# Optimization experiments

Hardware: AMD Instinct MI355X
Metric: run time of the kernel (lower is better)

## Reference

```python
import jax, jax.numpy as jnp
import numpy as np

B, S, D, H, F = 2, 4096, 512, 8, 2048
DH = D // H
EPS = 1e-3  # keras LayerNormalization default epsilon


def _ln(x, g, b):
    m = jnp.mean(x, axis=-1, keepdims=True)
    v = jnp.mean(jnp.square(x - m), axis=-1, keepdims=True)
    return (x - m) * jax.lax.rsqrt(v + EPS) * g + b


def setup_inputs() -> dict:
    key = jax.random.key(0)
    ks = jax.random.split(key, 8)
    sd = 0.02
    x = jax.random.normal(ks[0], (B, S, D), jnp.float32)
    # 0/1 additive-style mask: 1 above the diagonal -> masked via mask * -1e9 (causal)
    mask = jnp.triu(jnp.ones((S, S), jnp.float32), k=1)[None, None]
    return {
        "x": x,
        "mask": mask,
        "wq": jax.random.normal(ks[1], (D, D), jnp.float32) * sd, "bq": jnp.zeros((D,), jnp.float32),
        "wk": jax.random.normal(ks[2], (D, D), jnp.float32) * sd, "bk": jnp.zeros((D,), jnp.float32),
        "wv": jax.random.normal(ks[3], (D, D), jnp.float32) * sd, "bv": jnp.zeros((D,), jnp.float32),
        "wo": jax.random.normal(ks[4], (D, D), jnp.float32) * sd, "bo": jnp.zeros((D,), jnp.float32),
        "ln1_g": jnp.ones((D,), jnp.float32), "ln1_b": jnp.zeros((D,), jnp.float32),
        "w1": jax.random.normal(ks[5], (D, F), jnp.float32) * sd, "b1": jnp.zeros((F,), jnp.float32),
        "w2": jax.random.normal(ks[6], (F, D), jnp.float32) * sd, "b2": jnp.zeros((D,), jnp.float32),
        "ln2_g": jnp.ones((D,), jnp.float32), "ln2_b": jnp.zeros((D,), jnp.float32),
    }


def reference(x, mask, wq, bq, wk, bk, wv, bv, wo, bo, ln1_g, ln1_b,
              w1, b1, w2, b2, ln2_g, ln2_b):
    # --- multi-head attention (dropout = identity at inference) ---
    def heads(t, w, b):  # [B,S,D] -> [B,H,S,DH]
        return (t @ w + b).reshape(B, S, H, DH).transpose(0, 2, 1, 3)
    q = heads(x, wq, bq)
    k = heads(x, wk, bk)
    v = heads(x, wv, bv)
    scores = jnp.einsum("bhqd,bhkd->bhqk", q, k) / jnp.sqrt(jnp.float32(DH))
    scores = scores + mask * (-1e9)
    attn = jax.nn.softmax(scores, axis=-1)            # [B,H,S,S] -- the 1 GB tensor
    ctx = jnp.einsum("bhqk,bhkd->bhqd", attn, v)       # [B,H,S,DH]
    ctx = ctx.transpose(0, 2, 1, 3).reshape(B, S, D)
    attn_out = ctx @ wo + bo
    # --- residual + LN 1 ---
    y = _ln(x + attn_out, ln1_g, ln1_b)
    # --- pointwise FFN (Conv1D kernel_size=1 == Dense) ---
    ffn = jax.nn.relu(y @ w1 + b1) @ w2 + b2
    # --- residual + LN 2 ---
    return _ln(y + ffn, ln2_g, ln2_b)
```

## Files before the change

### kernel.cpp

```cpp
#include <hip/hip_runtime.h>
#include <hip/hip_bf16.h>
#include <math.h>

#define Bb 2
#define Ss 4096
#define Dd 512
#define Hh 8
#define Ff 2048
#define Mm 8192
#define QT3 1536
#define KVB 128

typedef float  f32x4  __attribute__((ext_vector_type(4)));
typedef short  bf16x8 __attribute__((ext_vector_type(8)));

__device__ __forceinline__ ushort f2bf(float f) {
  union { float f; uint u; } c; c.f = f;
  uint u = c.u;
  uint r = (u + 0x7fffu + ((u >> 16) & 1u)) >> 16;
  return (ushort)r;
}

__device__ __forceinline__ ushort f2bf_rhu(float f) {
  union { float f; uint u; } c; c.f = f;
  return (ushort)((c.u + 0x8000u) >> 16);
}

__device__ __forceinline__ void gload_lds16(const ushort* g, ushort* l) {
  __builtin_amdgcn_global_load_lds(
      (const __attribute__((address_space(1))) void*)g,
      (__attribute__((address_space(3))) void*)l, 16, 0, 0);
}

template<bool OUTBF, bool RELU>
__global__ __launch_bounds__(256) void gemm_mfma(const ushort* __restrict__ A,
                                                 const ushort* __restrict__ Bt,
                                                 const float* __restrict__ bias,
                                                 void* __restrict__ Cout,
                                                 int M, int N, int K) {
  __shared__ __align__(16) ushort As[128 * 32];
  __shared__ __align__(16) ushort Bs[128 * 32];
  const int t = threadIdx.x;
  const int w = t >> 6, lane = t & 63;
  const int lrow = lane & 15, lhi = lane >> 4;
  const int bm = blockIdx.y * 128, bn = blockIdx.x * 128;
  const int wm = (w >> 1) * 64, wn = (w & 1) * 64;
  const int sr = t >> 2, sc = (t & 3) * 8;

  f32x4 acc[4][4];
#pragma unroll
  for (int i = 0; i < 4; ++i)
#pragma unroll
    for (int j = 0; j < 4; ++j) acc[i][j] = (f32x4)(0.f);

  const ushort* Ap = A  + (size_t)(bm + sr) * K + sc;
  const ushort* Bp = Bt + (size_t)(bn + sr) * K + sc;
  const size_t rowK64 = (size_t)64 * K;
  ushort* AsW0 = As + w * 512;
  ushort* AsW1 = As + 2048 + w * 512;
  ushort* BsW0 = Bs + w * 512;
  ushort* BsW1 = Bs + 2048 + w * 512;

  for (int k0 = 0; k0 < K; k0 += 32) {
    __syncthreads();
    gload_lds16(Ap + k0,          AsW0);
    gload_lds16(Ap + rowK64 + k0, AsW1);
    gload_lds16(Bp + k0,          BsW0);
    gload_lds16(Bp + rowK64 + k0, BsW1);
    __syncthreads();
    bf16x8 af[4], bfr[4];
#pragma unroll
    for (int i = 0; i < 4; ++i)
      af[i] = *(const bf16x8*)&As[(wm + i * 16 + lrow) * 32 + lhi * 8];
#pragma unroll
    for (int j = 0; j < 4; ++j)
      bfr[j] = *(const bf16x8*)&Bs[(wn + j * 16 + lrow) * 32 + lhi * 8];
#pragma unroll
    for (int i = 0; i < 4; ++i)
#pragma unroll
      for (int j = 0; j < 4; ++j)
        acc[i][j] = __builtin_amdgcn_mfma_f32_16x16x32_bf16(af[i], bfr[j], acc[i][j], 0, 0, 0);
  }

  float bvs[4];
#pragma unroll
  for (int j = 0; j < 4; ++j) bvs[j] = bias[bn + wn + j * 16 + lrow];

#pragma unroll
  for (int i = 0; i < 4; ++i)
#pragma unroll
    for (int r = 0; r < 4; ++r) {
      const int row = bm + wm + i * 16 + lhi * 4 + r;
#pragma unroll
      for (int j = 0; j < 4; ++j) {
        float val = acc[i][j][r] + bvs[j];
        if (RELU) val = fmaxf(val, 0.f);
        const size_t idx = (size_t)row * N + bn + wn + j * 16 + lrow;
        if (OUTBF) ((ushort*)Cout)[idx] = f2bf(val);
        else       ((float*)Cout)[idx]  = val;
      }
    }
}

__global__ __launch_bounds__(256, 3) void flash_attn_mfma(const ushort* __restrict__ qkv,
                                                          ushort* __restrict__ ctx) {
  __shared__ __align__(16) ushort Ks[128][72];
  __shared__ __align__(16) ushort Vt[64][136];
  __shared__ __align__(16) ushort Ps[4][16][136];

  const int t = threadIdx.x;
  const int w = t >> 6, lane = t & 63;
  const int lrow = lane & 15, lhi = lane >> 4;
  const int qt = (int)(gridDim.x - 1 - blockIdx.x);
  const int bh = blockIdx.y;
  const int bb = bh >> 3, hh = bh & 7;
  const int q0 = qt * 64;
  const size_t baseq = (size_t)bb * Ss * QT3 + hh * 64;
  const ushort* qp = qkv + baseq;
  const ushort* kp = qkv + baseq + 512;
  const ushort* vp = qkv + baseq + 1024;

  const int krow = t >> 1, kd0 = (t & 1) * 32;
  const int vk0 = lane * 2, vd0 = w * 16;

  bf16x8 qa[2];
  {
    const ushort* qsrc = qp + (size_t)(q0 + w * 16 + lrow) * QT3;
    qa[0] = *(const bf16x8*)(qsrc + lhi * 8);
    qa[1] = *(const bf16x8*)(qsrc + 32 + lhi * 8);
  }

  float m2[4], lsum[4];
  f32x4 oacc[4];
#pragma unroll
  for (int r = 0; r < 4; ++r) { m2[r] = -INFINITY; lsum[r] = 0.f; }
#pragma unroll
  for (int g = 0; g < 4; ++g) oacc[g] = (f32x4)(0.f);

  const int nt = (qt + 2) >> 1;
  const float C2 = 0.18033688f;

  bf16x8 kr[4], va[2], vb[2];
  {
    const ushort* ksrc = kp + (size_t)krow * QT3 + kd0;
#pragma unroll
    for (int j = 0; j < 4; ++j) kr[j] = *(const bf16x8*)(ksrc + j * 8);
    const ushort* vsrc = vp + (size_t)vk0 * QT3 + vd0;
    va[0] = *(const bf16x8*)(vsrc);
    va[1] = *(const bf16x8*)(vsrc + 8);
    vb[0] = *(const bf16x8*)(vsrc + QT3);
    vb[1] = *(const bf16x8*)(vsrc + QT3 + 8);
  }

  for (int kt = 0; kt < nt; ++kt) {
    const int j0 = kt * KVB;

    __syncthreads();
#pragma unroll
    for (int j = 0; j < 4; ++j)
      *(bf16x8*)&Ks[krow][kd0 + j * 8] = kr[j];
#pragma unroll
    for (int i = 0; i < 8; ++i) {
      uint p0 = (uint)(ushort)va[0][i] | ((uint)(ushort)vb[0][i] << 16);
      uint p1 = (uint)(ushort)va[1][i] | ((uint)(ushort)vb[1][i] << 16);
      *(uint*)&Vt[vd0 + i][vk0]     = p0;
      *(uint*)&Vt[vd0 + 8 + i][vk0] = p1;
    }
    __syncthreads();

    if (kt + 1 < nt) {
      const int jn = j0 + KVB;
      const ushort* ksrc = kp + (size_t)(jn + krow) * QT3 + kd0;
#pragma unroll
      for (int j = 0; j < 4; ++j) kr[j] = *(const bf16x8*)(ksrc + j * 8);
      const ushort* vsrc = vp + (size_t)(jn + vk0) * QT3 + vd0;
      va[0] = *(const bf16x8*)(vsrc);
      va[1] = *(const bf16x8*)(vsrc + 8);
      vb[0] = *(const bf16x8*)(vsrc + QT3);
      vb[1] = *(const bf16x8*)(vsrc + QT3 + 8);
    }

    f32x4 sacc[8];
#pragma unroll
    for (int g = 0; g < 8; ++g) sacc[g] = (f32x4)(0.f);
#pragma unroll
    for (int g = 0; g < 8; ++g)
#pragma unroll
      for (int kk = 0; kk < 2; ++kk) {
        bf16x8 kb = *(const bf16x8*)&Ks[g * 16 + lrow][kk * 32 + lhi * 8];
        sacc[g] = __builtin_amdgcn_mfma_f32_16x16x32_bf16(qa[kk], kb, sacc[g], 0, 0, 0);
      }

    if (j0 + KVB - 1 > q0) {
#pragma unroll
      for (int g = 0; g < 8; ++g) {
        const int kcol = j0 + g * 16 + lrow;
#pragma unroll
        for (int r = 0; r < 4; ++r) {
          const int qrow = q0 + w * 16 + lhi * 4 + r;
          if (kcol > qrow) sacc[g][r] = -1e30f;
        }
      }
    }

    float pm[4];
#pragma unroll
    for (int r = 0; r < 4; ++r) {
      float m01 = fmaxf(sacc[0][r], sacc[1][r]);
      float m23 = fmaxf(sacc[2][r], sacc[3][r]);
      float m45 = fmaxf(sacc[4][r], sacc[5][r]);
      float m67 = fmaxf(sacc[6][r], sacc[7][r]);
      pm[r] = fmaxf(fmaxf(m01, m23), fmaxf(m45, m67));
    }
    bool ok = true;
#pragma unroll
    for (int r = 0; r < 4; ++r) ok = ok && (pm[r] * C2 <= m2[r] + 8.f);
    if (!__all(ok)) {
      float mt2[4], alpha[4];
#pragma unroll
      for (int r = 0; r < 4; ++r) mt2[r] = pm[r] * C2;
#pragma unroll
      for (int off = 1; off <= 8; off <<= 1)
#pragma unroll
        for (int r = 0; r < 4; ++r)
          mt2[r] = fmaxf(mt2[r], __shfl_xor(mt2[r], off));
#pragma unroll
      for (int r = 0; r < 4; ++r) {
        const float mn = fmaxf(m2[r], mt2[r]);
        alpha[r] = exp2f(m2[r] - mn);
        m2[r] = mn;
        lsum[r] *= alpha[r];
#pragma unroll
        for (int g = 0; g < 4; ++g) oacc[g][r] *= alpha[r];
      }
    }

#pragma unroll
    for (int g = 0; g < 8; ++g)
#pragma unroll
      for (int r = 0; r < 4; ++r) {
        const float p = exp2f(fmaf(sacc[g][r], C2, -m2[r]));
        lsum[r] += p;
        Ps[w][lhi * 4 + r][g * 16 + lrow] = f2bf_rhu(p);
      }

    bf16x8 pa[4];
#pragma unroll
    for (int kk = 0; kk < 4; ++kk)
      pa[kk] = *(const bf16x8*)&Ps[w][lrow][kk * 32 + lhi * 8];
#pragma unroll
    for (int g = 0; g < 4; ++g)
#pragma unroll
      for (int kk = 0; kk < 4; ++kk) {
        bf16x8 vbb = *(const bf16x8*)&Vt[g * 16 + lrow][kk * 32 + lhi * 8];
        oacc[g] = __builtin_amdgcn_mfma_f32_16x16x32_bf16(pa[kk], vbb, oacc[g], 0, 0, 0);
      }
  }

#pragma unroll
  for (int off = 1; off <= 8; off <<= 1)
#pragma unroll
    for (int r = 0; r < 4; ++r)
      lsum[r] += __shfl_xor(lsum[r], off);

  const size_t cbase = (size_t)bb * Ss * Dd + hh * 64;
#pragma unroll
  for (int r = 0; r < 4; ++r) {
    const float inv = 1.f / lsum[r];
    ushort* dst = ctx + cbase + (size_t)(q0 + w * 16 + lhi * 4 + r) * Dd;
#pragma unroll
    for (int g = 0; g < 4; ++g)
      dst[g * 16 + lrow] = f2bf(oacc[g][r] * inv);
  }
}

template<bool WB>
__global__ __launch_bounds__(128) void add_ln(const float* __restrict__ x,
                                              const float* __restrict__ a,
                                              const float* __restrict__ g,
                                              const float* __restrict__ bta,
                                              float* __restrict__ out,
                                              ushort* __restrict__ outb) {
  __shared__ float red[4];
  const int row = blockIdx.x;
  const int tid = threadIdx.x;
  const size_t off = (size_t)row * Dd + tid * 4;
  const float4 xv = *(const float4*)(x + off);
  const float4 av = *(const float4*)(a + off);
  float4 sv;
  sv.x = xv.x + av.x; sv.y = xv.y + av.y; sv.z = xv.z + av.z; sv.w = xv.w + av.w;
  float sum = sv.x + sv.y + sv.z + sv.w;
  float sq  = sv.x * sv.x + sv.y * sv.y + sv.z * sv.z + sv.w * sv.w;
#pragma unroll
  for (int o = 32; o >= 1; o >>= 1) {
    sum += __shfl_down(sum, o);
    sq  += __shfl_down(sq, o);
  }
  if ((tid & 63) == 0) { red[(tid >> 6) * 2] = sum; red[(tid >> 6) * 2 + 1] = sq; }
  __syncthreads();
  const float tot = red[0] + red[2];
  const float tsq = red[1] + red[3];
  const float invD = 1.f / 512.f;
  const float mean = tot * invD;
  const float var  = tsq * invD - mean * mean;
  const float rs   = rsqrtf(var + 1e-3f);
  const float4 gv = *(const float4*)(g + tid * 4);
  const float4 bv = *(const float4*)(bta + tid * 4);
  float4 ov;
  ov.x = (sv.x - mean) * rs * gv.x + bv.x;
  ov.y = (sv.y - mean) * rs * gv.y + bv.y;
  ov.z = (sv.z - mean) * rs * gv.z + bv.z;
  ov.w = (sv.w - mean) * rs * gv.w + bv.w;
  *(float4*)(out + off) = ov;
  if (WB) {
    ushort4 ob = {f2bf(ov.x), f2bf(ov.y), f2bf(ov.z), f2bf(ov.w)};
    *(ushort4*)(outb + off) = ob;
  }
}

__global__ __launch_bounds__(256) void cast_bf16(const float* __restrict__ in,
                                                 ushort* __restrict__ out, int n4) {
  const int i = blockIdx.x * 256 + threadIdx.x;
  if (i < n4) {
    const float4 vin = ((const float4*)in)[i];
    ushort4 o = {f2bf(vin.x), f2bf(vin.y), f2bf(vin.z), f2bf(vin.w)};
    ((ushort4*)out)[i] = o;
  }
}

__global__ __launch_bounds__(256) void transpose_cast(const float* __restrict__ W,
                                                      ushort* __restrict__ Wt,
                                                      int K, int N) {
  __shared__ float tile[32][33];
  const int bk = blockIdx.y * 32, bn = blockIdx.x * 32;
  const int tx = threadIdx.x & 31, ty = threadIdx.x >> 5;
#pragma unroll
  for (int i = 0; i < 32; i += 8)
    tile[ty + i][tx] = W[(size_t)(bk + ty + i) * N + bn + tx];
  __syncthreads();
#pragma unroll
  for (int i = 0; i < 32; i += 8)
    Wt[(size_t)(bn + ty + i) * K + bk + tx] = f2bf(tile[tx][ty + i]);
}

__global__ __launch_bounds__(256) void concat3(const float* __restrict__ a,
                                               const float* __restrict__ b,
                                               const float* __restrict__ c,
                                               float* __restrict__ o) {
  const int i = blockIdx.x * 256 + threadIdx.x;
  if (i < 512) o[i] = a[i];
  else if (i < 1024) o[i] = b[i - 512];
  else if (i < 1536) o[i] = c[i - 1024];
}

extern "C" void kernel_launch(void* const* d_in, const int* in_sizes, int n_in,
                              void* d_out, int out_size, void* d_ws, size_t ws_size,
                              hipStream_t stream) {
  (void)in_sizes; (void)n_in; (void)out_size; (void)ws_size;
  const float* x   = (const float*)d_in[0];
  const float* wq  = (const float*)d_in[2];
  const float* bq  = (const float*)d_in[3];
  const float* wk  = (const float*)d_in[4];
  const float* bk  = (const float*)d_in[5];
  const float* wv  = (const float*)d_in[6];
  const float* bvp = (const float*)d_in[7];
  const float* wo  = (const float*)d_in[8];
  const float* bo  = (const float*)d_in[9];
  const float* g1  = (const float*)d_in[10];
  const float* be1 = (const float*)d_in[11];
  const float* w1  = (const float*)d_in[12];
  const float* b1  = (const float*)d_in[13];
  const float* w2  = (const float*)d_in[14];
  const float* b2  = (const float*)d_in[15];
  const float* g2  = (const float*)d_in[16];
  const float* be2 = (const float*)d_in[17];
  float* out = (float*)d_out;

  const size_t SZ  = (size_t)Mm * Dd;
  const size_t WSZ = (size_t)Dd * Dd;
  const size_t W1SZ = (size_t)Dd * Ff;

  float* fp = (float*)d_ws;
  float* attn_out = fp;
  float* y        = fp + SZ;
  float* ffn2     = fp + 2 * SZ;
  ushort* ub   = (ushort*)(fp + 3 * SZ);
  ushort* xb    = ub;
  ushort* qkvb  = ub + SZ;
  ushort* ctxb  = ub + 4 * SZ;
  ushort* yb    = ub + 5 * SZ;
  ushort* ffn1b = ub + 6 * SZ;
  ushort* wqkvt = ub + 10 * SZ;
  ushort* wkt   = wqkvt + WSZ;
  ushort* wvt   = wkt + WSZ;
  ushort* wot   = wqkvt + 3 * WSZ;
  ushort* w1t   = wot + WSZ;
  ushort* w2t   = w1t + W1SZ;
  float*  bqkv  = (float*)(w2t + W1SZ);

  cast_bf16<<<dim3((int)(SZ / 4 / 256)), dim3(256), 0, stream>>>(x, xb, (int)(SZ / 4));
  transpose_cast<<<dim3(16, 16), dim3(256), 0, stream>>>(wq, wqkvt, Dd, Dd);
  transpose_cast<<<dim3(16, 16), dim3(256), 0, stream>>>(wk, wkt, Dd, Dd);
  transpose_cast<<<dim3(16, 16), dim3(256), 0, stream>>>(wv, wvt, Dd, Dd);
  transpose_cast<<<dim3(16, 16), dim3(256), 0, stream>>>(wo, wot, Dd, Dd);
  transpose_cast<<<dim3(64, 16), dim3(256), 0, stream>>>(w1, w1t, Dd, Ff);
  transpose_cast<<<dim3(16, 64), dim3(256), 0, stream>>>(w2, w2t, Ff, Dd);
  concat3<<<dim3(6), dim3(256), 0, stream>>>(bq, bk, bvp, bqkv);

  const dim3 blk(256);
  gemm_mfma<true,  false><<<dim3(12, 64), blk, 0, stream>>>(xb, wqkvt, bqkv, qkvb, Mm, QT3, Dd);
  flash_attn_mfma<<<dim3(64, 16), blk, 0, stream>>>(qkvb, ctxb);
  gemm_mfma<false, false><<<dim3(4, 64), blk, 0, stream>>>(ctxb, wot, bo, attn_out, Mm, Dd, Dd);
  add_ln<true><<<dim3(8192), dim3(128), 0, stream>>>(x, attn_out, g1, be1, y, yb);
  gemm_mfma<true,  true ><<<dim3(16, 64), blk, 0, stream>>>(yb, w1t, b1, ffn1b, Mm, Ff, Dd);
  gemm_mfma<false, false><<<dim3(4, 64), blk, 0, stream>>>(ffn1b, w2t, b2, ffn2, Mm, Dd, Ff);
  add_ln<false><<<dim3(8192), dim3(128), 0, stream>>>(y, ffn2, g2, be2, out, (ushort*)nullptr);
}
```

Before: 427.4 us.

## Split causal flash attention over KV chunks with a combine pass; use BM=64 tiles for N=512 GEMMs

The flash attention kernel now splits each query tile's causal KV range into chunks of up to 8 KV blocks, each handled by its own workgroup. Each workgroup writes unnormalized partial outputs plus its running max and sum. A new combine kernel merges these partials with log-sum-exp weights into the context tensor. This evens out the long tail from the triangular workload and adds parallelism, at the cost of extra partial writes and reads and one more launch. The GEMM kernel also gains a BM template parameter, and the N=512 output projection and FFN2 GEMMs use 64-row tiles to double their block count.

```diff
diff --git a/kernel.cpp b/kernel.cpp
--- a/kernel.cpp
+++ b/kernel.cpp
@@ -10,6 +10,7 @@
 #define Mm 8192
 #define QT3 1536
 #define KVB 128
+#define CSTEPS 8
 
 typedef float  f32x4  __attribute__((ext_vector_type(4)));
 typedef short  bf16x8 __attribute__((ext_vector_type(8)));
@@ -20,7 +21,9 @@
   uint r = (u + 0x7fffu + ((u >> 16) & 1u)) >> 16;
   return (ushort)r;
 }
-
+__device__ __forceinline__ float bf2f(ushort u) {
+  union { uint u; float f; } c; c.u = (uint)u << 16; return c.f;
+}
 __device__ __forceinline__ ushort f2bf_rhu(float f) {
   union { float f; uint u; } c; c.f = f;
   return (ushort)((c.u + 0x8000u) >> 16);
@@ -32,24 +35,25 @@
       (__attribute__((address_space(3))) void*)l, 16, 0, 0);
 }
 
-template<bool OUTBF, bool RELU>
+template<int BM, bool OUTBF, bool RELU>
 __global__ __launch_bounds__(256) void gemm_mfma(const ushort* __restrict__ A,
                                                  const ushort* __restrict__ Bt,
                                                  const float* __restrict__ bias,
                                                  void* __restrict__ Cout,
                                                  int M, int N, int K) {
-  __shared__ __align__(16) ushort As[128 * 32];
+  constexpr int MI = BM / 32;
+  __shared__ __align__(16) ushort As[BM * 32];
   __shared__ __align__(16) ushort Bs[128 * 32];
   const int t = threadIdx.x;
   const int w = t >> 6, lane = t & 63;
   const int lrow = lane & 15, lhi = lane >> 4;
-  const int bm = blockIdx.y * 128, bn = blockIdx.x * 128;
-  const int wm = (w >> 1) * 64, wn = (w & 1) * 64;
+  const int bm = blockIdx.y * BM, bn = blockIdx.x * 128;
+  const int wm = (w >> 1) * (BM / 2), wn = (w & 1) * 64;
   const int sr = t >> 2, sc = (t & 3) * 8;
 
-  f32x4 acc[4][4];
-#pragma unroll
-  for (int i = 0; i < 4; ++i)
+  f32x4 acc[MI][4];
+#pragma unroll
+  for (int i = 0; i < MI; ++i)
 #pragma unroll
     for (int j = 0; j < 4; ++j) acc[i][j] = (f32x4)(0.f);
 
@@ -63,20 +67,20 @@
 
   for (int k0 = 0; k0 < K; k0 += 32) {
     __syncthreads();
-    gload_lds16(Ap + k0,          AsW0);
-    gload_lds16(Ap + rowK64 + k0, AsW1);
+    gload_lds16(Ap + k0, AsW0);
+    if (BM == 128) gload_lds16(Ap + rowK64 + k0, AsW1);
     gload_lds16(Bp + k0,          BsW0);
     gload_lds16(Bp + rowK64 + k0, BsW1);
     __syncthreads();
-    bf16x8 af[4], bfr[4];
-#pragma unroll
-    for (int i = 0; i < 4; ++i)
+    bf16x8 af[MI], bfr[4];
+#pragma unroll
+    for (int i = 0; i < MI; ++i)
       af[i] = *(const bf16x8*)&As[(wm + i * 16 + lrow) * 32 + lhi * 8];
 #pragma unroll
     for (int j = 0; j < 4; ++j)
       bfr[j] = *(const bf16x8*)&Bs[(wn + j * 16 + lrow) * 32 + lhi * 8];
 #pragma unroll
-    for (int i = 0; i < 4; ++i)
+    for (int i = 0; i < MI; ++i)
 #pragma unroll
       for (int j = 0; j < 4; ++j)
         acc[i][j] = __builtin_amdgcn_mfma_f32_16x16x32_bf16(af[i], bfr[j], acc[i][j], 0, 0, 0);
@@ -87,7 +91,7 @@
   for (int j = 0; j < 4; ++j) bvs[j] = bias[bn + wn + j * 16 + lrow];
 
 #pragma unroll
-  for (int i = 0; i < 4; ++i)
+  for (int i = 0; i < MI; ++i)
 #pragma unroll
     for (int r = 0; r < 4; ++r) {
       const int row = bm + wm + i * 16 + lhi * 4 + r;
@@ -102,8 +106,10 @@
     }
 }
 
-__global__ __launch_bounds__(256, 3) void flash_attn_mfma(const ushort* __restrict__ qkv,
-                                                          ushort* __restrict__ ctx) {
+__global__ __launch_bounds__(256, 3) void flash_attn_split(const ushort* __restrict__ qkv,
+                                                           ushort* __restrict__ P_O,
+                                                           float* __restrict__ P_m,
+                                                           float* __restrict__ P_l) {
   __shared__ __align__(16) ushort Ks[128][72];
   __shared__ __align__(16) ushort Vt[64][136];
   __shared__ __align__(16) ushort Ps[4][16][136];
@@ -111,8 +117,13 @@
   const int t = threadIdx.x;
   const int w = t >> 6, lane = t & 63;
   const int lrow = lane & 15, lhi = lane >> 4;
-  const int qt = (int)(gridDim.x - 1 - blockIdx.x);
-  const int bh = blockIdx.y;
+  const int qt = 63 - (int)blockIdx.x;
+  const int bh = (int)blockIdx.y >> 2, cc = (int)blockIdx.y & 3;
+  const int nt_total = (qt + 2) >> 1;
+  const int s0 = cc * CSTEPS;
+  if (s0 >= nt_total) return;
+  const int s_end = min(nt_total, s0 + CSTEPS);
+
   const int bb = bh >> 3, hh = bh & 7;
   const int q0 = qt * 64;
   const size_t baseq = (size_t)bb * Ss * QT3 + hh * 64;
@@ -137,23 +148,22 @@
 #pragma unroll
   for (int g = 0; g < 4; ++g) oacc[g] = (f32x4)(0.f);
 
-  const int nt = (qt + 2) >> 1;
   const float C2 = 0.18033688f;
 
   bf16x8 kr[4], va[2], vb[2];
   {
-    const ushort* ksrc = kp + (size_t)krow * QT3 + kd0;
+    const ushort* ksrc = kp + (size_t)(s0 * KVB + krow) * QT3 + kd0;
 #pragma unroll
     for (int j = 0; j < 4; ++j) kr[j] = *(const bf16x8*)(ksrc + j * 8);
-    const ushort* vsrc = vp + (size_t)vk0 * QT3 + vd0;
+    const ushort* vsrc = vp + (size_t)(s0 * KVB + vk0) * QT3 + vd0;
     va[0] = *(const bf16x8*)(vsrc);
     va[1] = *(const bf16x8*)(vsrc + 8);
     vb[0] = *(const bf16x8*)(vsrc + QT3);
     vb[1] = *(const bf16x8*)(vsrc + QT3 + 8);
   }
 
-  for (int kt = 0; kt < nt; ++kt) {
-    const int j0 = kt * KVB;
+  for (int s = s0; s < s_end; ++s) {
+    const int j0 = s * KVB;
 
     __syncthreads();
 #pragma unroll
@@ -168,7 +178,7 @@
     }
     __syncthreads();
 
-    if (kt + 1 < nt) {
+    if (s + 1 < s_end) {
       const int jn = j0 + KVB;
       const ushort* ksrc = kp + (size_t)(jn + krow) * QT3 + kd0;
 #pragma unroll
@@ -216,7 +226,7 @@
 #pragma unroll
     for (int r = 0; r < 4; ++r) ok = ok && (pm[r] * C2 <= m2[r] + 8.f);
     if (!__all(ok)) {
-      float mt2[4], alpha[4];
+      float mt2[4];
 #pragma unroll
       for (int r = 0; r < 4; ++r) mt2[r] = pm[r] * C2;
 #pragma unroll
@@ -227,11 +237,11 @@
 #pragma unroll
       for (int r = 0; r < 4; ++r) {
         const float mn = fmaxf(m2[r], mt2[r]);
-        alpha[r] = exp2f(m2[r] - mn);
+        const float alpha = exp2f(m2[r] - mn);
         m2[r] = mn;
-        lsum[r] *= alpha[r];
-#pragma unroll
-        for (int g = 0; g < 4; ++g) oacc[g][r] *= alpha[r];
+        lsum[r] *= alpha;
+#pragma unroll
+        for (int g = 0; g < 4; ++g) oacc[g][r] *= alpha;
       }
     }
 
@@ -263,14 +273,53 @@
     for (int r = 0; r < 4; ++r)
       lsum[r] += __shfl_xor(lsum[r], off);
 
-  const size_t cbase = (size_t)bb * Ss * Dd + hh * 64;
+  const size_t pbase = ((size_t)(bh * 64 + qt) * 4 + cc) * 64;
 #pragma unroll
   for (int r = 0; r < 4; ++r) {
-    const float inv = 1.f / lsum[r];
-    ushort* dst = ctx + cbase + (size_t)(q0 + w * 16 + lhi * 4 + r) * Dd;
+    const int row = w * 16 + lhi * 4 + r;
+    ushort* dst = P_O + (pbase + row) * 64;
 #pragma unroll
     for (int g = 0; g < 4; ++g)
-      dst[g * 16 + lrow] = f2bf(oacc[g][r] * inv);
+      dst[g * 16 + lrow] = f2bf(oacc[g][r]);
+    if (lrow == 0) {
+      P_m[pbase + row] = m2[r];
+      P_l[pbase + row] = lsum[r];
+    }
+  }
+}
+
+__global__ __launch_bounds__(256) void flash_combine(const ushort* __restrict__ P_O,
+                                                     const float* __restrict__ P_m,
+                                                     const float* __restrict__ P_l,
+                                                     ushort* __restrict__ ctx) {
+  const int qt = blockIdx.x, bh = blockIdx.y;
+  const int bb = bh >> 3, hh = bh & 7;
+  const int nc = (((qt + 2) >> 1) + CSTEPS - 1) / CSTEPS;
+  const int t = threadIdx.x;
+  const int d = t & 63, rq = t >> 6;
+  const size_t pb = (size_t)(bh * 64 + qt) * 4;
+
+  for (int rr = 0; rr < 16; ++rr) {
+    const int row = rr * 4 + rq;
+    float m[4], l[4];
+    float mstar = -INFINITY;
+#pragma unroll
+    for (int c = 0; c < 4; ++c)
+      if (c < nc) {
+        m[c] = P_m[(pb + c) * 64 + row];
+        l[c] = P_l[(pb + c) * 64 + row];
+        mstar = fmaxf(mstar, m[c]);
+      }
+    float od = 0.f, ls = 0.f;
+#pragma unroll
+    for (int c = 0; c < 4; ++c)
+      if (c < nc) {
+        const float wc = exp2f(m[c] - mstar);
+        od += wc * bf2f(P_O[((pb + c) * 64 + row) * 64 + d]);
+        ls += wc * l[c];
+      }
+    const int sg = qt * 64 + row;
+    ctx[(size_t)bb * Ss * Dd + (size_t)sg * Dd + hh * 64 + d] = f2bf(od / ls);
   }
 }
 
@@ -397,6 +446,9 @@
   ushort* w1t   = wot + WSZ;
   ushort* w2t   = w1t + W1SZ;
   float*  bqkv  = (float*)(w2t + W1SZ);
+  float*  P_m   = bqkv + 2048;
+  float*  P_l   = P_m + 524288;
+  ushort* P_O   = ffn1b;
 
   cast_bf16<<<dim3((int)(SZ / 4 / 256)), dim3(256), 0, stream>>>(x, xb, (int)(SZ / 4));
   transpose_cast<<<dim3(16, 16), dim3(256), 0, stream>>>(wq, wqkvt, Dd, Dd);
@@ -408,11 +460,12 @@
   concat3<<<dim3(6), dim3(256), 0, stream>>>(bq, bk, bvp, bqkv);
 
   const dim3 blk(256);
-  gemm_mfma<true,  false><<<dim3(12, 64), blk, 0, stream>>>(xb, wqkvt, bqkv, qkvb, Mm, QT3, Dd);
-  flash_attn_mfma<<<dim3(64, 16), blk, 0, stream>>>(qkvb, ctxb);
-  gemm_mfma<false, false><<<dim3(4, 64), blk, 0, stream>>>(ctxb, wot, bo, attn_out, Mm, Dd, Dd);
+  gemm_mfma<128, true,  false><<<dim3(12, 64), blk, 0, stream>>>(xb, wqkvt, bqkv, qkvb, Mm, QT3, Dd);
+  flash_attn_split<<<dim3(64, 64), blk, 0, stream>>>(qkvb, P_O, P_m, P_l);
+  flash_combine<<<dim3(64, 16), blk, 0, stream>>>(P_O, P_m, P_l, ctxb);
+  gemm_mfma<64,  false, false><<<dim3(4, 128), blk, 0, stream>>>(ctxb, wot, bo, attn_out, Mm, Dd, Dd);
   add_ln<true><<<dim3(8192), dim3(128), 0, stream>>>(x, attn_out, g1, be1, y, yb);
-  gemm_mfma<true,  true ><<<dim3(16, 64), blk, 0, stream>>>(yb, w1t, b1, ffn1b, Mm, Ff, Dd);
-  gemm_mfma<false, false><<<dim3(4, 64), blk, 0, stream>>>(ffn1b, w2t, b2, ffn2, Mm, Dd, Ff);
+  gemm_mfma<128, true,  true ><<<dim3(16, 64), blk, 0, stream>>>(yb, w1t, b1, ffn1b, Mm, Ff, Dd);
+  gemm_mfma<64,  false, false><<<dim3(4, 128), blk, 0, stream>>>(ffn1b, w2t, b2, ffn2, Mm, Dd, Ff);
   add_ln<false><<<dim3(8192), dim3(128), 0, stream>>>(y, ffn2, g2, be2, out, (ushort*)nullptr);
 }
```

Measured after the change: 441.6 us. +3.3%, slower.
